# Kernel optimization log

Hardware: AMD Instinct MI355X
Metric: run time of the kernel (lower is better)

## Reference

```python
import jax, jax.numpy as jnp
from jax import lax
import numpy as np

B = 128
EPS = 1e-5


def _local_conv(x, w, b, kh, kw, sh, sw):
    # x: [B, C, H, W]; w: [nkh, nkw, O, C, kh, kw]; b: [O, nkh, nkw]
    nkh, nkw = w.shape[0], w.shape[1]
    # gather strided patches: [B, C, nkh, nkw, kh, kw]
    pats = jnp.stack([
        jnp.stack([
            x[:, :, di:di + sh * (nkh - 1) + 1:sh, dj:dj + sw * (nkw - 1) + 1:sw]
            for dj in range(kw)], axis=-1)
        for di in range(kh)], axis=-2)
    # per-location (unshared) contraction
    out = jnp.einsum('bchwkl,hwockl->bohw', pats, w)
    return out + b[None]


def _flatten_into_2d(o):
    # [B, O, h, w] -> [B, 1, r*h, r*w] with r = sqrt(O), channel-vector tiled as rxr block
    b, oc, h, w = o.shape
    r = int(round(oc ** 0.5))
    y = o.transpose(0, 2, 3, 1).reshape(b, h, w, r, r)
    y = y.transpose(0, 1, 3, 2, 4).reshape(b, r * h, r * w)
    return y[:, None]


def _layernorm2d(x, g, bta):
    # normalize over last two dims (torch nn.LayerNorm([H, W]))
    m = jnp.mean(x, axis=(-2, -1), keepdims=True)
    v = jnp.mean((x - m) ** 2, axis=(-2, -1), keepdims=True)
    return (x - m) * lax.rsqrt(v + EPS) * g + bta


def _maxpool2(x):
    return lax.reduce_window(x, -jnp.inf, lax.max, (1, 1, 2, 2), (1, 1, 2, 2), 'VALID')


def setup_inputs() -> dict:
    key = jax.random.key(0)
    ks = jax.random.split(key, 5)
    x = jax.random.normal(ks[0], (B, 3, 224, 224), jnp.float32)
    # xavier-normal-ish std for each per-location weight
    w0 = jax.random.normal(ks[1], (55, 55, 16, 3, 8, 8), jnp.float32) * 0.0406
    b0 = jnp.zeros((16, 55, 55), jnp.float32)
    g0 = jnp.ones((220, 220), jnp.float32)
    be0 = jnp.zeros((220, 220), jnp.float32)
    w1 = jax.random.normal(ks[2], (53, 53, 9, 1, 6, 6), jnp.float32) * 0.074
    b1 = jnp.zeros((9, 53, 53), jnp.float32)
    g1 = jnp.ones((159, 159), jnp.float32)
    be1 = jnp.zeros((159, 159), jnp.float32)
    fcw = jax.random.normal(ks[3], (1000, 25281), jnp.float32) * 0.01
    fcb = jnp.zeros((1000,), jnp.float32)
    return {"x": x, "w0": w0, "b0": b0, "g0": g0, "be0": be0,
            "w1": w1, "b1": b1, "g1": g1, "be1": be1, "fcw": fcw, "fcb": fcb}


def reference(x, w0, b0, g0, be0, w1, b1, g1, be1, fcw, fcb):
    # layer 0 (locally connected, padding 0): [B,16,55,55] -> 2D map [B,1,220,220]
    h = _local_conv(x, w0, b0, 8, 8, 4, 4)
    h = _flatten_into_2d(h)
    h = _layernorm2d(jax.nn.relu(h), g0, be0)
    h = _maxpool2(h)  # [B,1,110,110]  (i==0 -> pool; dropout is identity in eval)
    # layer 1: [B,9,53,53] -> [B,1,159,159]; i==1 odd -> no pool
    h = _local_conv(h, w1, b1, 6, 6, 2, 2)
    h = _flatten_into_2d(h)
    h = _layernorm2d(jax.nn.relu(h), g1, be1)
    logits = h.reshape(h.shape[0], -1) @ fcw.T + fcb
    return jax.nn.softmax(logits, axis=1)
```

## Files before the change

kernel.cpp:

```cpp
#include <hip/hip_runtime.h>


typedef __attribute__((ext_vector_type(8))) short short8;
typedef __attribute__((ext_vector_type(4))) float float4v;

__device__ __forceinline__ short f2bf(float f) {
    unsigned u = __float_as_uint(f);
    u += 0x7FFFu + ((u >> 16) & 1u);
    return (short)(u >> 16);
}

__global__ __launch_bounds__(256) void k_conv0(const float* __restrict__ x,
                                               const float* __restrict__ w0,
                                               const float* __restrict__ b0,
                                               float* __restrict__ y0)
{
    __shared__ float wl[2][192 * 20];
    const int g = threadIdx.x >> 7;
    const int t = threadIdx.x & 127;
    int loc = blockIdx.x * 2 + g;
    const bool active = (loc < 3025);
    if (!active) loc = 3024;
    const int oh = loc / 55, ow = loc % 55;
    const float* wbase = w0 + loc * 3072;

    #pragma unroll
    for (int i = 0; i < 6; ++i) {
        int q   = t + (i << 7);
        int o_r = q & 15;
        int kq  = q >> 4;
        float4 wv = *(const float4*)(wbase + o_r * 192 + (kq << 2));
        wl[g][(kq * 4 + 0) * 20 + o_r] = wv.x;
        wl[g][(kq * 4 + 1) * 20 + o_r] = wv.y;
        wl[g][(kq * 4 + 2) * 20 + o_r] = wv.z;
        wl[g][(kq * 4 + 3) * 20 + o_r] = wv.w;
    }
    __syncthreads();

    const int oP = t & 3;
    const int bP = t >> 2;
    float acc[4][4] = {};

    const float* xloc = x + (oh << 2) * 224 + (ow << 2);

    #pragma unroll 2
    for (int c = 0; c < 48; ++c) {
        const int ch  = c >> 4;
        const int rw  = (c >> 1) & 7;
        const int col = (c & 1) << 2;
        const float* xp = xloc + (ch * 224 + rw) * 224 + col;
        float4 xq[4];
        #pragma unroll
        for (int i2 = 0; i2 < 4; ++i2)
            xq[i2] = *(const float4*)(xp + (((bP << 2) + i2) * 3) * 50176);
        float wv[4][4];
        #pragma unroll
        for (int u = 0; u < 4; ++u) {
            float4 wq = *(const float4*)&wl[g][((c << 2) + u) * 20 + (oP << 2)];
            wv[u][0] = wq.x; wv[u][1] = wq.y; wv[u][2] = wq.z; wv[u][3] = wq.w;
        }
        #pragma unroll
        for (int i2 = 0; i2 < 4; ++i2) {
            const float xr[4] = {xq[i2].x, xq[i2].y, xq[i2].z, xq[i2].w};
            #pragma unroll
            for (int u = 0; u < 4; ++u)
                #pragma unroll
                for (int j = 0; j < 4; ++j)
                    acc[i2][j] += xr[u] * wv[u][j];
        }
    }

    if (active) {
        #pragma unroll
        for (int i2 = 0; i2 < 4; ++i2) {
            int b = (bP << 2) + i2;
            float4 outv;
            float ov[4];
            #pragma unroll
            for (int j = 0; j < 4; ++j) {
                float v = acc[i2][j] + b0[((oP << 2) + j) * 3025 + loc];
                ov[j] = v > 0.f ? v : 0.f;
            }
            outv.x = ov[0]; outv.y = ov[1]; outv.z = ov[2]; outv.w = ov[3];
            *(float4*)(y0 + b * 48400 + ((oh << 2) + oP) * 220 + (ow << 2)) = outv;
        }
    }
}

__global__ void k_stats(const float* __restrict__ src, float2* __restrict__ stats, int count)
{
    const int b = blockIdx.x, t = threadIdx.x;
    const float* p = src + (long)b * count;
    const int nq = count >> 2;
    float s = 0.f, s2 = 0.f;
    for (int i = t; i < nq; i += 256) {
        float4 v = *(const float4*)(p + (i << 2));
        s  += (v.x + v.y) + (v.z + v.w);
        s2 += (v.x * v.x + v.y * v.y) + (v.z * v.z + v.w * v.w);
    }
    if (t == 0 && (count & 3)) {
        for (int i = nq << 2; i < count; ++i) { float v = p[i]; s += v; s2 += v * v; }
    }
    #pragma unroll
    for (int off = 32; off > 0; off >>= 1) {
        s  += __shfl_down(s,  off, 64);
        s2 += __shfl_down(s2, off, 64);
    }
    __shared__ float rs[4], rs2[4];
    if ((t & 63) == 0) { rs[t >> 6] = s; rs2[t >> 6] = s2; }
    __syncthreads();
    if (t == 0) {
        float S  = rs[0] + rs[1] + rs[2] + rs[3];
        float S2 = rs2[0] + rs2[1] + rs2[2] + rs2[3];
        float m  = S / count;
        float var = S2 / count - m * m;
        stats[b] = make_float2(m, rsqrtf(var + 1e-5f));
    }
}

__global__ void k_pool(const float* __restrict__ y0, const float2* __restrict__ st,
                       const float* __restrict__ g0, const float* __restrict__ be0,
                       float* __restrict__ P)
{
    int idx = blockIdx.x * 256 + threadIdx.x;
    if (idx >= 128 * 110 * 110) return;
    int b = idx / 12100, r = idx % 12100;
    int ph = r / 110, pw = r % 110;
    float2 s = st[b];
    int gb = (ph * 220 + pw) * 2;
    const float* yb = y0 + b * 48400 + gb;
    float2 a0 = *(const float2*)yb;
    float2 a1 = *(const float2*)(yb + 220);
    float2 ga0 = *(const float2*)(g0 + gb),  ga1 = *(const float2*)(g0 + gb + 220);
    float2 ba0 = *(const float2*)(be0 + gb), ba1 = *(const float2*)(be0 + gb + 220);
    float n0 = (a0.x - s.x) * s.y * ga0.x + ba0.x;
    float n1 = (a0.y - s.x) * s.y * ga0.y + ba0.y;
    float n2 = (a1.x - s.x) * s.y * ga1.x + ba1.x;
    float n3 = (a1.y - s.x) * s.y * ga1.y + ba1.y;
    P[idx] = fmaxf(fmaxf(n0, n1), fmaxf(n2, n3));
}

__global__ __launch_bounds__(128) void k_conv1(const float* __restrict__ P,
                                               const float* __restrict__ w1,
                                               const float* __restrict__ b1,
                                               float* __restrict__ y1)
{
    __shared__ float wloc[324];
    __shared__ float pat[128 * 64];
    const int t = threadIdx.x;
    const int loc = blockIdx.x;
    const int oh = loc / 53, ow = loc % 53;
    for (int e = t; e < 324; e += 128) wloc[e] = w1[loc * 324 + e];
    #pragma unroll
    for (int i = 0; i < 9; ++i) {
        int q = t + (i << 7);
        int b_r = q / 9, c = q % 9;
        float pv[4];
        #pragma unroll
        for (int u = 0; u < 4; ++u) {
            int sidx = (c << 2) + u;
            int ki = sidx / 6, kj = sidx % 6;
            pv[u] = P[b_r * 12100 + ((oh << 1) + ki) * 110 + (ow << 1) + kj];
        }
        float4 pq; pq.x = pv[0]; pq.y = pv[1]; pq.z = pv[2]; pq.w = pv[3];
        *(float4*)&pat[(b_r << 6) + ((c ^ (b_r & 15)) << 2)] = pq;
    }
    __syncthreads();
    const int b = t;
    float acc[9];
    #pragma unroll
    for (int o = 0; o < 9; ++o) acc[o] = b1[o * 2809 + loc];
    #pragma unroll
    for (int s4 = 0; s4 < 9; ++s4) {
        float4 pq = *(const float4*)&pat[(b << 6) + ((s4 ^ (b & 15)) << 2)];
        #pragma unroll
        for (int o = 0; o < 9; ++o) {
            float4 wq = *(const float4*)&wloc[o * 36 + (s4 << 2)];
            acc[o] += pq.x * wq.x + pq.y * wq.y + pq.z * wq.z + pq.w * wq.w;
        }
    }
    #pragma unroll
    for (int o = 0; o < 9; ++o) {
        float v = acc[o] > 0.f ? acc[o] : 0.f;
        y1[b * 25281 + (3 * oh + o / 3) * 159 + 3 * ow + o % 3] = v;
    }
}

__global__ void k_normb(const float* __restrict__ y1, const float2* __restrict__ st,
                        const float* __restrict__ g1, const float* __restrict__ be1,
                        unsigned short* __restrict__ hb)
{
    int idx = blockIdx.x * 256 + threadIdx.x;
    int b = idx / 25600, k = idx % 25600;
    float v = 0.f;
    if (k < 25281) {
        float2 s = st[b];
        v = (y1[b * 25281 + k] - s.x) * s.y * g1[k] + be1[k];
    }
    hb[idx] = (unsigned short)f2bf(v);
}

__global__ __launch_bounds__(256) void k_fc_mfma(const unsigned short* __restrict__ hb,
                                                 const float* __restrict__ fcw,
                                                 float* __restrict__ pp)
{
    const int lane = threadIdx.x & 63;
    const int wave = threadIdx.x >> 6;
    const int n0   = (blockIdx.x << 6) + (wave << 4);
    const int k0   = blockIdx.y << 9;
    const int m16  = lane & 15;
    const int q    = lane >> 4;
    const int nc   = n0 + m16;
    const int nrow = nc < 1000 ? nc : 999;
    const long wrow = (long)nrow * 25281;

    float4v acc[8];
    #pragma unroll
    for (int i = 0; i < 8; ++i) acc[i] = (float4v){0.f, 0.f, 0.f, 0.f};

    const unsigned short* ha = hb + m16 * 25600;

    for (int c = 0; c < 16; ++c) {
        const int kb = k0 + (c << 5) + (q << 3);
        long widx = wrow + kb;
        short8 bf;
        if (widx + 8 <= 25281000L) {
            #pragma unroll
            for (int j = 0; j < 8; ++j) bf[j] = f2bf(fcw[widx + j]);
        } else {
            #pragma unroll
            for (int j = 0; j < 8; ++j) {
                long e = widx + j;
                bf[j] = f2bf(e < 25281000L ? fcw[e] : 0.f);
            }
        }
        #pragma unroll
        for (int mt = 0; mt < 8; ++mt) {
            short8 af = *(const short8*)(ha + mt * 16 * 25600 + kb);
            acc[mt] = __builtin_amdgcn_mfma_f32_16x16x32_bf16(af, bf, acc[mt], 0, 0, 0);
        }
    }

    float* prow = pp + ((size_t)blockIdx.y << 17);
    #pragma unroll
    for (int mt = 0; mt < 8; ++mt) {
        const int mb = (mt << 4) + (q << 2);
        #pragma unroll
        for (int i = 0; i < 4; ++i)
            prow[(size_t)(mb + i) * 1024 + nc] = acc[mt][i];
    }
}

__global__ void k_softmax(const float* __restrict__ partials, const float* __restrict__ fcb,
                          float* __restrict__ out)
{
    const int b = blockIdx.x, t = threadIdx.x;
    float v[4];
    float mx = -3.4e38f;
    #pragma unroll
    for (int i = 0; i < 4; ++i) {
        int o = t + (i << 8);
        float s = -3.4e38f;
        if (o < 1000) {
            s = fcb[o];
            for (int bz = 0; bz < 50; ++bz)
                s += partials[(((bz << 7) + b) << 10) + o];
        }
        v[i] = s;
        mx = fmaxf(mx, s);
    }
    __shared__ float red[4], red2[4];
    #pragma unroll
    for (int off = 32; off > 0; off >>= 1) mx = fmaxf(mx, __shfl_down(mx, off, 64));
    if ((t & 63) == 0) red[t >> 6] = mx;
    __syncthreads();
    float M = fmaxf(fmaxf(red[0], red[1]), fmaxf(red[2], red[3]));
    float se = 0.f;
    #pragma unroll
    for (int i = 0; i < 4; ++i) {
        int o = t + (i << 8);
        if (o < 1000) { v[i] = expf(v[i] - M); se += v[i]; }
    }
    #pragma unroll
    for (int off = 32; off > 0; off >>= 1) se += __shfl_down(se, off, 64);
    if ((t & 63) == 0) red2[t >> 6] = se;
    __syncthreads();
    float inv = 1.f / (red2[0] + red2[1] + red2[2] + red2[3]);
    #pragma unroll
    for (int i = 0; i < 4; ++i) {
        int o = t + (i << 8);
        if (o < 1000) out[b * 1000 + o] = v[i] * inv;
    }
}

extern "C" void kernel_launch(void* const* d_in, const int* in_sizes, int n_in,
                              void* d_out, int out_size, void* d_ws, size_t ws_size,
                              hipStream_t stream)
{
    const float* x   = (const float*)d_in[0];
    const float* w0  = (const float*)d_in[1];
    const float* b0  = (const float*)d_in[2];
    const float* g0  = (const float*)d_in[3];
    const float* be0 = (const float*)d_in[4];
    const float* w1  = (const float*)d_in[5];
    const float* b1  = (const float*)d_in[6];
    const float* g1  = (const float*)d_in[7];
    const float* be1 = (const float*)d_in[8];
    const float* fcw = (const float*)d_in[9];
    const float* fcb = (const float*)d_in[10];
    float* out = (float*)d_out;
    float* ws  = (float*)d_ws;

    float*  y0  = ws;
    float2* st0 = (float2*)(ws + 6195200);
    float*  P   = ws + 6195456;
    float*  y1  = ws + 7744256;
    float2* st1 = (float2*)(ws + 10980224);
    unsigned short* hb = (unsigned short*)(ws + 10980480);
    float*  pp  = ws;

    hipLaunchKernelGGL(k_conv0,   dim3(1513),    dim3(256), 0, stream, x, w0, b0, y0);
    hipLaunchKernelGGL(k_stats,   dim3(128),     dim3(256), 0, stream, y0, st0, 48400);
    hipLaunchKernelGGL(k_pool,    dim3(6050),    dim3(256), 0, stream, y0, st0, g0, be0, P);
    hipLaunchKernelGGL(k_conv1,   dim3(2809),    dim3(128), 0, stream, P, w1, b1, y1);
    hipLaunchKernelGGL(k_stats,   dim3(128),     dim3(256), 0, stream, y1, st1, 25281);
    hipLaunchKernelGGL(k_normb,   dim3(12800),   dim3(256), 0, stream, y1, st1, g1, be1, hb);
    hipLaunchKernelGGL(k_fc_mfma, dim3(16, 50),  dim3(256), 0, stream, hb, fcw, pp);
    hipLaunchKernelGGL(k_softmax, dim3(128),     dim3(256), 0, stream, pp, fcb, out);
}
```

Before: 498.3 us.

## Tile conv0 over five adjacent locations with double-buffered LDS staging

The first locally connected layer now gives each block five horizontally adjacent output locations and stages the overlapping input rows in shared memory. This lets a single input row load serve several locations, cutting redundant global reads. Input and weight tiles are double-buffered in LDS with register prefetch of the next row, and block IDs are remapped across XCDs for locality. The cost is fewer blocks (605), more registers per thread and idle lanes, since only some thread groups own the fifth location.

```diff
diff --git a/kernel.cpp b/kernel.cpp
--- a/kernel.cpp
+++ b/kernel.cpp
@@ -10,79 +10,120 @@
     return (short)(u >> 16);
 }
 
-__global__ __launch_bounds__(256) void k_conv0(const float* __restrict__ x,
-                                               const float* __restrict__ w0,
-                                               const float* __restrict__ b0,
-                                               float* __restrict__ y0)
-{
-    __shared__ float wl[2][192 * 20];
-    const int g = threadIdx.x >> 7;
-    const int t = threadIdx.x & 127;
-    int loc = blockIdx.x * 2 + g;
-    const bool active = (loc < 3025);
-    if (!active) loc = 3024;
-    const int oh = loc / 55, ow = loc % 55;
-    const float* wbase = w0 + loc * 3072;
-
-    #pragma unroll
-    for (int i = 0; i < 6; ++i) {
-        int q   = t + (i << 7);
-        int o_r = q & 15;
-        int kq  = q >> 4;
-        float4 wv = *(const float4*)(wbase + o_r * 192 + (kq << 2));
-        wl[g][(kq * 4 + 0) * 20 + o_r] = wv.x;
-        wl[g][(kq * 4 + 1) * 20 + o_r] = wv.y;
-        wl[g][(kq * 4 + 2) * 20 + o_r] = wv.z;
-        wl[g][(kq * 4 + 3) * 20 + o_r] = wv.w;
-    }
-    __syncthreads();
-
-    const int oP = t & 3;
-    const int bP = t >> 2;
-    float acc[4][4] = {};
-
-    const float* xloc = x + (oh << 2) * 224 + (ow << 2);
+__global__ __launch_bounds__(256, 4) void k_conv0(const float* __restrict__ x,
+                                                  const float* __restrict__ w0,
+                                                  const float* __restrict__ b0,
+                                                  float* __restrict__ y0)
+{
+    __shared__ float xs[2][24 * 132];
+    __shared__ float wsd[2][640];
+
+    const int t = threadIdx.x;
+    const int orig = blockIdx.x;
+    const int xcd = orig & 7, lin = orig >> 3;
+    const int bid = (xcd < 5 ? xcd * 76 : 380 + (xcd - 5) * 75) + lin;
+    const int oh = bid / 11;
+    const int tw = bid - oh * 11;
+    const int ow0 = tw * 5;
+
+    const float* xrow0 = x + (oh << 2) * 224 + tw * 20;
+    const float* wbase = w0 + (oh * 55 + ow0) * 3072;
+
+    int sb[3], sc[3];
+    #pragma unroll
+    for (int i = 0; i < 3; ++i) {
+        int q = t + (i << 8);
+        sb[i] = q / 6;
+        sc[i] = q - sb[i] * 6;
+    }
+    const int  wlm  = t >> 5;
+    const int  wom  = (t & 31) >> 1;
+    const int  whm  = t & 1;
+    const bool wact = (t < 160);
+
+    const int bq = t & 31;
+    const int oq = (t >> 5) & 3;
+    const int lp = t >> 7;
+
+    float4 xv[3];
+    float4 wv = make_float4(0.f, 0.f, 0.f, 0.f);
+    #pragma unroll
+    for (int i = 0; i < 3; ++i)
+        xv[i] = *(const float4*)(xrow0 + sb[i] * 150528 + (sc[i] << 2));
+    if (wact)
+        wv = *(const float4*)(wbase + wlm * 3072 + wom * 192 + (whm << 2));
+
+    float acc[3][4][4] = {};
 
     #pragma unroll 2
-    for (int c = 0; c < 48; ++c) {
-        const int ch  = c >> 4;
-        const int rw  = (c >> 1) & 7;
-        const int col = (c & 1) << 2;
-        const float* xp = xloc + (ch * 224 + rw) * 224 + col;
-        float4 xq[4];
-        #pragma unroll
-        for (int i2 = 0; i2 < 4; ++i2)
-            xq[i2] = *(const float4*)(xp + (((bP << 2) + i2) * 3) * 50176);
-        float wv[4][4];
-        #pragma unroll
-        for (int u = 0; u < 4; ++u) {
-            float4 wq = *(const float4*)&wl[g][((c << 2) + u) * 20 + (oP << 2)];
-            wv[u][0] = wq.x; wv[u][1] = wq.y; wv[u][2] = wq.z; wv[u][3] = wq.w;
-        }
-        #pragma unroll
-        for (int i2 = 0; i2 < 4; ++i2) {
-            const float xr[4] = {xq[i2].x, xq[i2].y, xq[i2].z, xq[i2].w};
-            #pragma unroll
-            for (int u = 0; u < 4; ++u)
+    for (int k = 0; k < 24; ++k) {
+        float* xb = xs[k & 1];
+        float* wb = wsd[k & 1];
+        #pragma unroll
+        for (int i = 0; i < 3; ++i) {
+            float* d = xb + (sc[i] << 2) * 132 + sb[i];
+            d[0] = xv[i].x; d[132] = xv[i].y; d[264] = xv[i].z; d[396] = xv[i].w;
+        }
+        if (wact) {
+            float* d = wb + (wlm << 7) + (whm << 6) + wom;
+            d[0] = wv.x; d[16] = wv.y; d[32] = wv.z; d[48] = wv.w;
+        }
+        if (k < 23) {
+            const int kn = k + 1;
+            const int ch = kn >> 3, rw = kn & 7;
+            const float* xr = xrow0 + ch * 50176 + rw * 224;
+            #pragma unroll
+            for (int i = 0; i < 3; ++i)
+                xv[i] = *(const float4*)(xr + sb[i] * 150528 + (sc[i] << 2));
+            if (wact)
+                wv = *(const float4*)(wbase + wlm * 3072 + wom * 192
+                                      + (ch << 6) + (rw << 3) + (whm << 2));
+        }
+        __syncthreads();
+        #pragma unroll
+        for (int i = 0; i < 3; ++i) {
+            const int l = lp * 3 + i;
+            if (l < 5) {
                 #pragma unroll
-                for (int j = 0; j < 4; ++j)
-                    acc[i2][j] += xr[u] * wv[u][j];
-        }
-    }
-
-    if (active) {
-        #pragma unroll
-        for (int i2 = 0; i2 < 4; ++i2) {
-            int b = (bP << 2) + i2;
-            float4 outv;
-            float ov[4];
-            #pragma unroll
-            for (int j = 0; j < 4; ++j) {
-                float v = acc[i2][j] + b0[((oP << 2) + j) * 3025 + loc];
-                ov[j] = v > 0.f ? v : 0.f;
+                for (int kc = 0; kc < 8; ++kc) {
+                    float4 xq = *(const float4*)(xb + ((l << 2) + kc) * 132 + (bq << 2));
+                    float4 wq = *(const float4*)(wb + (l << 7) + (kc << 4) + (oq << 2));
+                    const float xr4[4] = {xq.x, xq.y, xq.z, xq.w};
+                    const float wr4[4] = {wq.x, wq.y, wq.z, wq.w};
+                    #pragma unroll
+                    for (int b4 = 0; b4 < 4; ++b4)
+                        #pragma unroll
+                        for (int j = 0; j < 4; ++j)
+                            acc[i][b4][j] += xr4[b4] * wr4[j];
+                }
             }
-            outv.x = ov[0]; outv.y = ov[1]; outv.z = ov[2]; outv.w = ov[3];
-            *(float4*)(y0 + b * 48400 + ((oh << 2) + oP) * 220 + (ow << 2)) = outv;
+        }
+    }
+
+    #pragma unroll
+    for (int i = 0; i < 3; ++i) {
+        const int l = lp * 3 + i;
+        if (l < 5) {
+            const int ow  = ow0 + l;
+            const int loc = oh * 55 + ow;
+            float bias[4];
+            #pragma unroll
+            for (int j = 0; j < 4; ++j)
+                bias[j] = b0[((oq << 2) + j) * 3025 + loc];
+            float* ybase = y0 + ((oh << 2) + oq) * 220 + (ow << 2);
+            #pragma unroll
+            for (int b4 = 0; b4 < 4; ++b4) {
+                const int b = (bq << 2) + b4;
+                float ov[4];
+                #pragma unroll
+                for (int j = 0; j < 4; ++j) {
+                    float v = acc[i][b4][j] + bias[j];
+                    ov[j] = v > 0.f ? v : 0.f;
+                }
+                float4 o4;
+                o4.x = ov[0]; o4.y = ov[1]; o4.z = ov[2]; o4.w = ov[3];
+                *(float4*)(ybase + b * 48400) = o4;
+            }
         }
     }
 }
@@ -319,7 +360,7 @@
     unsigned short* hb = (unsigned short*)(ws + 10980480);
     float*  pp  = ws;
 
-    hipLaunchKernelGGL(k_conv0,   dim3(1513),    dim3(256), 0, stream, x, w0, b0, y0);
+    hipLaunchKernelGGL(k_conv0,   dim3(605),     dim3(256), 0, stream, x, w0, b0, y0);
     hipLaunchKernelGGL(k_stats,   dim3(128),     dim3(256), 0, stream, y0, st0, 48400);
     hipLaunchKernelGGL(k_pool,    dim3(6050),    dim3(256), 0, stream, y0, st0, g0, be0, P);
     hipLaunchKernelGGL(k_conv1,   dim3(2809),    dim3(128), 0, stream, P, w1, b1, y1);
```

Measured after the change: 579.2 us. 16.2% more time.
